# Kernel tuning notes

Hardware: AMD Instinct MI355X
Metric: run time of the kernel (lower is better)

Reference implementation:

```python
import jax, jax.numpy as jnp
from jax import lax
import numpy as np

D_MODEL, N_STATES, N_GROUPS, K_CONV = 1024, 16, 8, 4
BATCH, LENGTH = 2, 2048


def setup_inputs() -> dict:
    key = jax.random.key(0)
    ks = jax.random.split(key, 8)
    x = jax.random.normal(ks[0], (BATCH, LENGTH, D_MODEL), dtype=jnp.float32)
    in_proj_w = jax.random.normal(ks[1], (2 * D_MODEL, D_MODEL), dtype=jnp.float32) * 0.02
    in_proj_b = jnp.zeros((2 * D_MODEL,), dtype=jnp.float32)
    delta_proj_w = jax.random.uniform(ks[2], (D_MODEL, D_MODEL), dtype=jnp.float32, minval=0.001, maxval=0.1)
    a_log = jnp.log(jnp.tile(jnp.arange(1, N_STATES + 1, dtype=jnp.float32), (D_MODEL, 1)))
    b_proj_w = jax.random.normal(ks[3], (N_GROUPS * N_STATES, D_MODEL), dtype=jnp.float32) * 1e-4
    b_proj_b = jnp.zeros((N_GROUPS * N_STATES,), dtype=jnp.float32)
    c_param = jax.random.normal(ks[4], (D_MODEL, N_STATES), dtype=jnp.float32) * 0.02
    # depthwise conv (groups = d_model): kernel [D, 1, K]
    conv_w = jax.random.normal(ks[5], (D_MODEL, 1, K_CONV), dtype=jnp.float32) * (1.0 / np.sqrt(K_CONV))
    conv_b = jnp.zeros((D_MODEL,), dtype=jnp.float32)
    return {"x": x, "in_proj_w": in_proj_w, "in_proj_b": in_proj_b,
            "delta_proj_w": delta_proj_w, "a_log": a_log,
            "b_proj_w": b_proj_w, "b_proj_b": b_proj_b, "c_param": c_param,
            "conv_w": conv_w, "conv_b": conv_b}


def _causal_conv(u, conv_w, conv_b):
    # u: [B, L, D] -> depthwise causal conv along L
    D = u.shape[-1]
    K = conv_w.shape[-1]
    uc = jnp.transpose(u, (0, 2, 1))  # [B, D, L]
    uc = lax.conv_general_dilated(uc, conv_w, window_strides=(1,),
                                  padding=[(K - 1, 0)], feature_group_count=D,
                                  dimension_numbers=("NCH", "OIH", "NCH"))
    uc = uc + conv_b[None, :, None]
    return jnp.transpose(uc, (0, 2, 1))  # [B, L, D]


def _selective_scan(delta, A, Bmat, c_param, u):
    # delta,u: [B,L,D]; A: [D,N]; Bmat: [B,L,G,N]; c_param: [D,N]
    Bsz, L, D = delta.shape
    N = A.shape[1]
    G = Bmat.shape[2]
    Bexp = jnp.repeat(Bmat, D // G, axis=2)            # [B,L,D,N]
    dA = jnp.exp(delta[..., None] * A)                  # [B,L,D,N]
    dBu = (delta * u)[..., None] * Bexp                 # [B,L,D,N]

    def step(h, xs):
        da, dbu = xs
        h = da * h + dbu                                # [B,D,N]
        y = jnp.einsum("bdn,dn->bd", h, c_param)
        return h, y

    h0 = jnp.zeros((Bsz, D, N), dtype=delta.dtype)
    _, ys = lax.scan(step, h0, (jnp.moveaxis(dA, 1, 0), jnp.moveaxis(dBu, 1, 0)))
    return jnp.moveaxis(ys, 0, 1)                       # [B,L,D]


def reference(x, in_proj_w, in_proj_b, delta_proj_w, a_log, b_proj_w, b_proj_b, c_param, conv_w, conv_b):
    Bsz, L, _ = x.shape
    N = a_log.shape[1]
    G = b_proj_w.shape[0] // N
    xp = x @ in_proj_w.T + in_proj_b                    # [B,L,2D]
    u, v = jnp.split(xp, 2, axis=-1)
    delta = jax.nn.softplus(u @ delta_proj_w.T)         # [B,L,D]
    A = -jnp.exp(a_log)                                 # [D,N]
    Bmat = (u @ b_proj_w.T + b_proj_b).reshape(Bsz, L, G, N)
    u_conv = jax.nn.silu(_causal_conv(u, conv_w, conv_b))
    y = _selective_scan(delta, A, Bmat, c_param, u_conv)
    return y * jax.nn.silu(v)
```

## Files before the change

kernel.cpp:

```cpp
#include <hip/hip_runtime.h>
#include <math.h>

#define LTOT 2048
#define MROWS 4096
#define CHK 64
#define NCH (LTOT / CHK)
#define SPAD 20

typedef short bf16x8 __attribute__((ext_vector_type(8)));
typedef float f32x4  __attribute__((ext_vector_type(4)));

__device__ __forceinline__ unsigned short bf16_rne(float f) {
  unsigned u = __float_as_uint(f);
  u += 0x7FFF + ((u >> 16) & 1);
  return (unsigned short)(u >> 16);
}
__device__ __forceinline__ float bf16_to_f(unsigned short h) {
  return __uint_as_float(((unsigned)h) << 16);
}
__device__ __forceinline__ float softplus_f(float x) {
  return (x > 15.f) ? x : log1pf(expf(x));
}
__device__ __forceinline__ float silu_f(float x) {
  return x / (1.f + expf(-x));
}

__global__ void k_cvt_all(const float* __restrict__ x, const float* __restrict__ w1,
                          const float* __restrict__ dw, const float* __restrict__ bw,
                          unsigned short* __restrict__ xh, unsigned short* __restrict__ xl,
                          unsigned short* __restrict__ wfh, unsigned short* __restrict__ wfl,
                          unsigned short* __restrict__ wdbAh, unsigned short* __restrict__ wdbAl) {
  const int blk = blockIdx.x;
  const float* src; unsigned short *h, *l; int i;
  if (blk < 4096)      { src = x;  h = xh;  l = xl;  i = blk * 256 + threadIdx.x; }
  else if (blk < 6144) { src = w1; h = wfh; l = wfl; i = (blk - 4096) * 256 + threadIdx.x; }
  else if (blk < 7168) { src = dw; h = wdbAh; l = wdbAl; i = (blk - 6144) * 256 + threadIdx.x; }
  else                 { src = bw; h = wdbAh + (size_t)1024*1024; l = wdbAl + (size_t)1024*1024;
                         i = (blk - 7168) * 256 + threadIdx.x; }
  const float4 v = ((const float4*)src)[i];
  ushort4 hh, ll;
  hh.x = bf16_rne(v.x); ll.x = bf16_rne(v.x - bf16_to_f(hh.x));
  hh.y = bf16_rne(v.y); ll.y = bf16_rne(v.y - bf16_to_f(hh.y));
  hh.z = bf16_rne(v.z); ll.z = bf16_rne(v.z - bf16_to_f(hh.z));
  hh.w = bf16_rne(v.w); ll.w = bf16_rne(v.w - bf16_to_f(hh.w));
  ((ushort4*)h)[i] = hh;
  ((ushort4*)l)[i] = ll;
}

__global__ __launch_bounds__(256) void k_cvt_t(const float* __restrict__ w1,
    unsigned short* __restrict__ th, unsigned short* __restrict__ tl) {
  __shared__ float ts[64][65];
  const int t = threadIdx.x;
  const int j0 = blockIdx.y * 64, k0 = blockIdx.x * 64;
  const int r = t >> 4, c4 = (t & 15) * 4;
  #pragma unroll
  for (int p = 0; p < 4; ++p) {
    const int row = p * 16 + r;
    const float4 v = *(const float4*)&w1[(size_t)(j0 + row) * 1024 + k0 + c4];
    ts[row][c4] = v.x; ts[row][c4+1] = v.y; ts[row][c4+2] = v.z; ts[row][c4+3] = v.w;
  }
  __syncthreads();
  #pragma unroll
  for (int p = 0; p < 4; ++p) {
    const int rk = p * 16 + r;
    ushort4 hh, ll;
    float f;
    f = ts[c4+0][rk]; hh.x = bf16_rne(f); ll.x = bf16_rne(f - bf16_to_f(hh.x));
    f = ts[c4+1][rk]; hh.y = bf16_rne(f); ll.y = bf16_rne(f - bf16_to_f(hh.y));
    f = ts[c4+2][rk]; hh.z = bf16_rne(f); ll.z = bf16_rne(f - bf16_to_f(hh.z));
    f = ts[c4+3][rk]; hh.w = bf16_rne(f); ll.w = bf16_rne(f - bf16_to_f(hh.w));
    *(ushort4*)&th[(size_t)(k0 + rk) * 1024 + j0 + c4] = hh;
    *(ushort4*)&tl[(size_t)(k0 + rk) * 1024 + j0 + c4] = ll;
  }
}

__global__ void k_bias(const float* __restrict__ b1, const float* __restrict__ dw,
                       const float* __restrict__ bw, const float* __restrict__ bb,
                       float* __restrict__ bfull) {
  const int t = threadIdx.x;
  const int j = blockIdx.x * 16 + (t >> 4);
  const int lane16 = t & 15;
  const float* W = (j < 1024) ? (dw + (size_t)j * 1024) : (bw + (size_t)(j - 1024) * 1024);
  float s = 0.f;
  for (int i = 0; i < 64; ++i) {
    const int k = lane16 + i * 16;
    s = fmaf(b1[k], W[k], s);
  }
  s += __shfl_xor(s, 8, 16);
  s += __shfl_xor(s, 4, 16);
  s += __shfl_xor(s, 2, 16);
  s += __shfl_xor(s, 1, 16);
  if (lane16 == 0) bfull[j] = s + ((j >= 1024) ? bb[j - 1024] : 0.f);
}

__global__ __launch_bounds__(256) void k_wcomp2(
    const unsigned short* __restrict__ Ah_g, const unsigned short* __restrict__ Al_g,
    const unsigned short* __restrict__ Bh_g, const unsigned short* __restrict__ Bl_g,
    unsigned short* __restrict__ outh, unsigned short* __restrict__ outl) {
  __shared__ __align__(16) unsigned short LAh[128*32];
  __shared__ __align__(16) unsigned short LAl[128*32];
  __shared__ __align__(16) unsigned short LBh[128*32];
  __shared__ __align__(16) unsigned short LBl[128*32];
  const int t = threadIdx.x;
  const int wave = t >> 6, lane = t & 63;
  const int m0 = blockIdx.y * 128;
  const int n0 = blockIdx.x * 128;
  const int wr = wave >> 1, wc = wave & 1;
  const int ln = lane & 15, kq = lane >> 4;
  const int srow = lane >> 2, scol = (lane & 3) * 8;

  f32x4 acc[4][4];
  #pragma unroll
  for (int i = 0; i < 4; ++i)
    #pragma unroll
    for (int j = 0; j < 4; ++j) acc[i][j] = (f32x4){0.f, 0.f, 0.f, 0.f};

  const unsigned short* pAh = Ah_g + (size_t)m0 * 1024;
  const unsigned short* pAl = Al_g + (size_t)m0 * 1024;
  const unsigned short* pBh = Bh_g + (size_t)n0 * 1024;
  const unsigned short* pBl = Bl_g + (size_t)n0 * 1024;

  auto stage = [&](const unsigned short* g, unsigned short* lds, int k0) {
    #pragma unroll
    for (int r = 0; r < 2; ++r) {
      const unsigned short* gp = g + (size_t)(r * 64 + wave * 16 + srow) * 1024 + k0 + scol;
      unsigned short* lp = lds + (r * 64 + wave * 16) * 32;
      __builtin_amdgcn_global_load_lds((const __attribute__((address_space(1))) void*)gp,
                                       (__attribute__((address_space(3))) void*)lp, 16, 0, 0);
    }
  };

  for (int k0 = 0; k0 < 1024; k0 += 32) {
    __syncthreads();
    stage(pAh, LAh, k0);
    stage(pAl, LAl, k0);
    stage(pBh, LBh, k0);
    stage(pBl, LBl, k0);
    __syncthreads();
    bf16x8 ah[4], al[4], bh[4], bl[4];
    #pragma unroll
    for (int i = 0; i < 4; ++i) {
      const int ar = (wr * 64 + i * 16 + ln) * 32 + kq * 8;
      const int br = (wc * 64 + i * 16 + ln) * 32 + kq * 8;
      ah[i] = *(const bf16x8*)&LAh[ar];
      al[i] = *(const bf16x8*)&LAl[ar];
      bh[i] = *(const bf16x8*)&LBh[br];
      bl[i] = *(const bf16x8*)&LBl[br];
    }
    #pragma unroll
    for (int i = 0; i < 4; ++i)
      #pragma unroll
      for (int j = 0; j < 4; ++j) {
        acc[i][j] = __builtin_amdgcn_mfma_f32_16x16x32_bf16(ah[i], bh[j], acc[i][j], 0, 0, 0);
        acc[i][j] = __builtin_amdgcn_mfma_f32_16x16x32_bf16(ah[i], bl[j], acc[i][j], 0, 0, 0);
        acc[i][j] = __builtin_amdgcn_mfma_f32_16x16x32_bf16(al[i], bh[j], acc[i][j], 0, 0, 0);
      }
  }

  const int rbase = (blockIdx.y < 8) ? 2176 : 1024;
  #pragma unroll
  for (int nj = 0; nj < 4; ++nj) {
    const int kcol = n0 + wc * 64 + nj * 16 + ln;
    #pragma unroll
    for (int mi = 0; mi < 4; ++mi) {
      const int i = m0 + wr * 64 + mi * 16 + kq * 4;
      #pragma unroll
      for (int j = 0; j < 4; ++j) {
        const float f = acc[mi][nj][j];
        const unsigned short hh = bf16_rne(f);
        const unsigned short ll = bf16_rne(f - bf16_to_f(hh));
        outh[(size_t)(rbase + i + j) * 1024 + kcol] = hh;
        outl[(size_t)(rbase + i + j) * 1024 + kcol] = ll;
      }
    }
  }
}

__global__ __launch_bounds__(256) void k_mm(
    const unsigned short* __restrict__ xh, const unsigned short* __restrict__ xl,
    const unsigned short* __restrict__ wfh, const unsigned short* __restrict__ wfl,
    const float* __restrict__ b1, const float* __restrict__ bfull,
    float* __restrict__ u_, float* __restrict__ v_,
    float* __restrict__ delta, float* __restrict__ Bm) {
  __shared__ __align__(16) unsigned short LAh[128*32];
  __shared__ __align__(16) unsigned short LAl[128*32];
  __shared__ __align__(16) unsigned short LBh[128*32];
  __shared__ __align__(16) unsigned short LBl[128*32];
  const int t = threadIdx.x;
  const int wave = t >> 6, lane = t & 63;
  const int wr = wave >> 1, wc = wave & 1;
  const int ln = lane & 15, kq = lane >> 4;
  const int srow = lane >> 2, scol = (lane & 3) * 8;
  const int flat = blockIdx.x;

  f32x4 acc[4][4];
  #pragma unroll
  for (int i = 0; i < 4; ++i)
    #pragma unroll
    for (int j = 0; j < 4; ++j) acc[i][j] = (f32x4){0.f, 0.f, 0.f, 0.f};

  if (flat < 256) {
    const int wg = (flat & 7) * 32 + (flat >> 3);
    const int tn = wg & 7;
    const int m0 = (wg >> 3) * 128;
    const unsigned short* pAh = xh + (size_t)m0 * 1024;
    const unsigned short* pAl = xl + (size_t)m0 * 1024;
    const unsigned short* pBh = wfh + (size_t)(2176 + tn * 128) * 1024;
    const unsigned short* pBl = wfl + (size_t)(2176 + tn * 128) * 1024;

    auto stage = [&](const unsigned short* g, unsigned short* lds, int k0) {
      #pragma unroll
      for (int r = 0; r < 2; ++r) {
        const unsigned short* gp = g + (size_t)(r * 64 + wave * 16 + srow) * 1024 + k0 + scol;
        unsigned short* lp = lds + (r * 64 + wave * 16) * 32;
        __builtin_amdgcn_global_load_lds((const __attribute__((address_space(1))) void*)gp,
                                         (__attribute__((address_space(3))) void*)lp, 16, 0, 0);
      }
    };

    for (int k0 = 0; k0 < 1024; k0 += 32) {
      __syncthreads();
      stage(pAh, LAh, k0);
      stage(pAl, LAl, k0);
      stage(pBh, LBh, k0);
      stage(pBl, LBl, k0);
      __syncthreads();
      bf16x8 ah[4], al[4], bh[4], bl[4];
      #pragma unroll
      for (int i = 0; i < 4; ++i) {
        const int ar = (wr * 64 + i * 16 + ln) * 32 + kq * 8;
        const int br = (wc * 64 + i * 16 + ln) * 32 + kq * 8;
        ah[i] = *(const bf16x8*)&LAh[ar];
        al[i] = *(const bf16x8*)&LAl[ar];
        bh[i] = *(const bf16x8*)&LBh[br];
        bl[i] = *(const bf16x8*)&LBl[br];
      }
      #pragma unroll
      for (int i = 0; i < 4; ++i)
        #pragma unroll
        for (int j = 0; j < 4; ++j) {
          acc[i][j] = __builtin_amdgcn_mfma_f32_16x16x32_bf16(ah[i], bh[j], acc[i][j], 0, 0, 0);
          acc[i][j] = __builtin_amdgcn_mfma_f32_16x16x32_bf16(ah[i], bl[j], acc[i][j], 0, 0, 0);
          acc[i][j] = __builtin_amdgcn_mfma_f32_16x16x32_bf16(al[i], bh[j], acc[i][j], 0, 0, 0);
        }
    }

    #pragma unroll
    for (int nj = 0; nj < 4; ++nj) {
      const int colg = tn * 128 + wc * 64 + nj * 16 + ln;
      const float bv = bfull[colg];
      #pragma unroll
      for (int mi = 0; mi < 4; ++mi) {
        const int row = m0 + wr * 64 + mi * 16 + kq * 4;
        #pragma unroll
        for (int j = 0; j < 4; ++j)
          delta[(size_t)(row + j) * 1024 + colg] = softplus_f(acc[mi][nj][j] + bv);
      }
    }
  } else {
    const int f2 = flat - 256;
    const int wg = (f2 & 7) * 68 + (f2 >> 3);
    const int tn = wg % 17;
    const int m0 = (wg / 17) * 128;
    const unsigned short* pAh = xh + (size_t)m0 * 1024;
    const unsigned short* pBh = wfh + (size_t)(tn * 128) * 1024;

    auto stage = [&](const unsigned short* g, unsigned short* lds, int k0) {
      #pragma unroll
      for (int r = 0; r < 2; ++r) {
        const unsigned short* gp = g + (size_t)(r * 64 + wave * 16 + srow) * 1024 + k0 + scol;
        unsigned short* lp = lds + (r * 64 + wave * 16) * 32;
        __builtin_amdgcn_global_load_lds((const __attribute__((address_space(1))) void*)gp,
                                         (__attribute__((address_space(3))) void*)lp, 16, 0, 0);
      }
    };

    for (int k0 = 0; k0 < 1024; k0 += 32) {
      __syncthreads();
      stage(pAh, LAh, k0);
      stage(pBh, LBh, k0);
      __syncthreads();
      bf16x8 ah[4], bh[4];
      #pragma unroll
      for (int i = 0; i < 4; ++i) {
        const int ar = (wr * 64 + i * 16 + ln) * 32 + kq * 8;
        const int br = (wc * 64 + i * 16 + ln) * 32 + kq * 8;
        ah[i] = *(const bf16x8*)&LAh[ar];
        bh[i] = *(const bf16x8*)&LBh[br];
      }
      #pragma unroll
      for (int i = 0; i < 4; ++i)
        #pragma unroll
        for (int j = 0; j < 4; ++j)
          acc[i][j] = __builtin_amdgcn_mfma_f32_16x16x32_bf16(ah[i], bh[j], acc[i][j], 0, 0, 0);
    }

    #pragma unroll
    for (int nj = 0; nj < 4; ++nj) {
      const int colg = tn * 128 + wc * 64 + nj * 16 + ln;
      const float bv = (tn < 16) ? b1[colg] : bfull[1024 + colg - 2048];
      #pragma unroll
      for (int mi = 0; mi < 4; ++mi) {
        const int row = m0 + wr * 64 + mi * 16 + kq * 4;
        #pragma unroll
        for (int j = 0; j < 4; ++j) {
          const float val = acc[mi][nj][j] + bv;
          if (tn < 8)       u_[(size_t)(row + j) * 1024 + colg] = val;
          else if (tn < 16) v_[(size_t)(row + j) * 1024 + colg - 1024] = val;
          else              Bm[(size_t)(row + j) * 128 + colg - 2048] = val;
        }
      }
    }
  }
}

__global__ __launch_bounds__(256) void k_scanA(
    const float* __restrict__ delta, const float* __restrict__ u_,
    const float* __restrict__ Bm, const float* __restrict__ a_log,
    const float* __restrict__ cw, const float* __restrict__ cb,
    float* __restrict__ hend, float* __restrict__ Pp)
{
  __shared__ float sru[68][SPAD];
  __shared__ float sd[CHK][SPAD];
  __shared__ float sb[CHK][SPAD];
  __shared__ float suc[CHK][SPAD];
  const int t = threadIdx.x;
  const int bid = blockIdx.x;
  const int dblk = bid & 63;
  const int ch   = (bid >> 6) & (NCH - 1);
  const int b    = bid >> 11;
  const int d0 = dblk * 16;
  const int g  = dblk >> 3;
  const int l0 = ch * CHK;
  const size_t mb = (size_t)b * LTOT;

  {
    const int lrow = t >> 2;
    const int lc4  = (t & 3) * 4;
    const size_t r = mb + l0 + lrow;
    float4 rd = *(const float4*)&delta[r*1024 + d0 + lc4];
    float4 rb = *(const float4*)&Bm[r*128 + g*16 + lc4];
    *(float4*)&sd[lrow][lc4] = rd;
    *(float4*)&sb[lrow][lc4] = rb;
    const int sl = l0 + lrow - 4;
    float4 ru = (sl >= 0) ? *(const float4*)&u_[(mb + sl)*1024 + d0 + lc4]
                          : (float4){0.f, 0.f, 0.f, 0.f};
    *(float4*)&sru[lrow][lc4] = ru;
    if (t < 16) {
      const int rr2 = 64 + (t >> 2);
      const int sl2 = l0 + rr2 - 4;
      float4 r2 = *(const float4*)&u_[(mb + sl2)*1024 + d0 + (t & 3) * 4];
      *(float4*)&sru[rr2][(t & 3) * 4] = r2;
    }
  }
  __syncthreads();
  {
    const int c = t & 15;
    const int rb4 = (t >> 4) * 4;
    const float4 cwf = *(const float4*)&cw[(d0 + c) * 4];
    const float cbf = cb[d0 + c];
    #pragma unroll
    for (int q = 0; q < 4; ++q) {
      const int l = rb4 + q;
      float a = cbf;
      a = fmaf(sru[l+1][c], cwf.x, a);
      a = fmaf(sru[l+2][c], cwf.y, a);
      a = fmaf(sru[l+3][c], cwf.z, a);
      a = fmaf(sru[l+4][c], cwf.w, a);
      suc[l][c] = silu_f(a);
    }
  }
  __syncthreads();

  const int gi = t >> 4;
  const int n  = t & 15;
  const int d  = d0 + gi;
  const float A2 = -expf(a_log[d*16 + n]) * 1.4426950408889634f;

  float h = 0.f, P = 1.f;
  #pragma unroll 8
  for (int l = 0; l < CHK; ++l) {
    const float dv = sd[l][gi];
    const float uv = suc[l][gi];
    const float bv = sb[l][n];
    const float da = exp2f(dv * A2);
    P *= da;
    h = fmaf(da, h, dv * uv * bv);
  }
  const size_t idx = ((size_t)(b*NCH + ch) * 1024 + d) * 16 + n;
  hend[idx] = h;
  Pp[idx]   = P;
}

__global__ void k_scanB(float* hP, const float* __restrict__ Pp)
{
  const int t = blockIdx.x * 256 + threadIdx.x;
  const int b  = t >> 14;
  const int dn = t & 16383;
  float H = 0.f;
  for (int ch = 0; ch < NCH; ++ch) {
    const size_t idx = ((size_t)(b*NCH + ch) << 14) + dn;
    const float he = hP[idx];
    const float P  = Pp[idx];
    hP[idx] = H;
    H = fmaf(P, H, he);
  }
}

__global__ __launch_bounds__(256) void k_scanC(
    const float* __restrict__ v_, const float* __restrict__ delta,
    const float* __restrict__ u_, const float* __restrict__ Bm,
    const float* __restrict__ a_log, const float* __restrict__ cp,
    const float* __restrict__ cw, const float* __restrict__ cb,
    const float* __restrict__ Hstart, float* __restrict__ out)
{
  __shared__ float sru[68][SPAD];
  __shared__ float sd[CHK][SPAD];
  __shared__ float sb[CHK][SPAD];
  __shared__ float suc[CHK][SPAD];
  __shared__ float sv[CHK][SPAD];
  __shared__ float sy[CHK][SPAD];
  const int t = threadIdx.x;
  const int bid = blockIdx.x;
  const int dblk = bid & 63;
  const int ch   = (bid >> 6) & (NCH - 1);
  const int b    = bid >> 11;
  const int d0 = dblk * 16;
  const int g  = dblk >> 3;
  const int l0 = ch * CHK;
  const size_t mb = (size_t)b * LTOT;

  {
    const int lrow = t >> 2;
    const int lc4  = (t & 3) * 4;
    const size_t r = mb + l0 + lrow;
    float4 rd = *(const float4*)&delta[r*1024 + d0 + lc4];
    float4 rb = *(const float4*)&Bm[r*128 + g*16 + lc4];
    float4 rv = *(const float4*)&v_[r*1024 + d0 + lc4];
    *(float4*)&sd[lrow][lc4] = rd;
    *(float4*)&sb[lrow][lc4] = rb;
    *(float4*)&sv[lrow][lc4] = rv;
    const int sl = l0 + lrow - 4;
    float4 ru = (sl >= 0) ? *(const float4*)&u_[(mb + sl)*1024 + d0 + lc4]
                          : (float4){0.f, 0.f, 0.f, 0.f};
    *(float4*)&sru[lrow][lc4] = ru;
    if (t < 16) {
      const int rr2 = 64 + (t >> 2);
      const int sl2 = l0 + rr2 - 4;
      float4 r2 = *(const float4*)&u_[(mb + sl2)*1024 + d0 + (t & 3) * 4];
      *(float4*)&sru[rr2][(t & 3) * 4] = r2;
    }
  }
  __syncthreads();
  {
    const int c = t & 15;
    const int rb4 = (t >> 4) * 4;
    const float4 cwf = *(const float4*)&cw[(d0 + c) * 4];
    const float cbf = cb[d0 + c];
    #pragma unroll
    for (int q = 0; q < 4; ++q) {
      const int l = rb4 + q;
      float a = cbf;
      a = fmaf(sru[l+1][c], cwf.x, a);
      a = fmaf(sru[l+2][c], cwf.y, a);
      a = fmaf(sru[l+3][c], cwf.z, a);
      a = fmaf(sru[l+4][c], cwf.w, a);
      suc[l][c] = silu_f(a);
    }
  }
  __syncthreads();

  const int gi = t >> 4;
  const int n  = t & 15;
  const int d  = d0 + gi;
  const float A2 = -expf(a_log[d*16 + n]) * 1.4426950408889634f;
  const float cc = cp[d*16 + n];
  float h = Hstart[((size_t)(b*NCH + ch) * 1024 + d) * 16 + n];

  #pragma unroll
  for (int l16 = 0; l16 < CHK; l16 += 16) {
    float p[16];
    #pragma unroll
    for (int j = 0; j < 16; ++j) {
      const int l = l16 + j;
      const float dv = sd[l][gi];
      const float uv = suc[l][gi];
      const float bv = sb[l][n];
      const float da = exp2f(dv * A2);
      h = fmaf(da, h, dv * uv * bv);
      p[j] = h * cc;
    }
    float q8[8];
    #pragma unroll
    for (int j = 0; j < 8; ++j) {
      const float send = (n & 8) ? p[j]     : p[j + 8];
      const float keep = (n & 8) ? p[j + 8] : p[j];
      q8[j] = keep + __shfl_xor(send, 8, 16);
    }
    float q4[4];
    #pragma unroll
    for (int j = 0; j < 4; ++j) {
      const float send = (n & 4) ? q8[j]     : q8[j + 4];
      const float keep = (n & 4) ? q8[j + 4] : q8[j];
      q4[j] = keep + __shfl_xor(send, 4, 16);
    }
    float q2[2];
    #pragma unroll
    for (int j = 0; j < 2; ++j) {
      const float send = (n & 2) ? q4[j]     : q4[j + 2];
      const float keep = (n & 2) ? q4[j + 2] : q4[j];
      q2[j] = keep + __shfl_xor(send, 2, 16);
    }
    {
      const float send = (n & 1) ? q2[0] : q2[1];
      const float keep = (n & 1) ? q2[1] : q2[0];
      sy[l16 + n][gi] = keep + __shfl_xor(send, 1, 16);
    }
  }

  __syncthreads();
  const int rr = t >> 4;
  const int c  = t & 15;
  #pragma unroll
  for (int k = 0; k < 4; ++k) {
    const int r = rr + k * 16;
    const float vv = sv[r][c];
    out[(mb + l0 + r) * 1024 + d0 + c] = sy[r][c] * silu_f(vv);
  }
}

extern "C" void kernel_launch(void* const* d_in, const int* in_sizes, int n_in,
                              void* d_out, int out_size, void* d_ws, size_t ws_size,
                              hipStream_t stream) {
  const float* x    = (const float*)d_in[0];
  const float* w1   = (const float*)d_in[1];
  const float* b1   = (const float*)d_in[2];
  const float* dw   = (const float*)d_in[3];
  const float* alog = (const float*)d_in[4];
  const float* bw   = (const float*)d_in[5];
  const float* bb   = (const float*)d_in[6];
  const float* cp   = (const float*)d_in[7];
  const float* cw   = (const float*)d_in[8];
  const float* cb   = (const float*)d_in[9];
  float* out = (float*)d_out;

  const size_t M4 = (size_t)MROWS * 1024;
  float* u_    = (float*)d_ws;
  float* v_    = u_ + M4;
  float* delta = v_ + M4;
  float* Bm    = delta + M4;
  unsigned short* xh  = (unsigned short*)(Bm + (size_t)MROWS * 128);
  unsigned short* xl  = xh + M4;
  unsigned short* wfh = xl + M4;
  unsigned short* wfl = wfh + (size_t)3200 * 1024;
  float* bfull = (float*)(wfl + (size_t)3200 * 1024);
  unsigned short* wdbAh = (unsigned short*)delta;
  unsigned short* wdbAl = wdbAh + (size_t)1152 * 1024;
  unsigned short* w1th  = wdbAl + (size_t)1152 * 1024;
  unsigned short* w1tl  = w1th + (size_t)1024 * 1024;
  float* hend = (float*)wfh;
  float* Pp   = hend + (size_t)2 * NCH * 1024 * 16;

  k_cvt_all<<<7296, 256, 0, stream>>>(x, w1, dw, bw, xh, xl, wfh, wfl, wdbAh, wdbAl);
  k_cvt_t<<<dim3(16, 16), 256, 0, stream>>>(w1, w1th, w1tl);
  k_bias<<<72, 256, 0, stream>>>(b1, dw, bw, bb, bfull);
  k_wcomp2<<<dim3(8, 9), 256, 0, stream>>>(wdbAh, wdbAl, w1th, w1tl, wfh, wfl);
  k_mm<<<800, 256, 0, stream>>>(xh, xl, wfh, wfl, b1, bfull, u_, v_, delta, Bm);
  k_scanA<<<2 * NCH * 64, 256, 0, stream>>>(delta, u_, Bm, alog, cw, cb, hend, Pp);
  k_scanB<<<128, 256, 0, stream>>>(hend, Pp);
  k_scanC<<<2 * NCH * 64, 256, 0, stream>>>(v_, delta, u_, Bm, alog, cp, cw, cb, hend, out);
}
```

Before: 217.7 us.

## Drop split-bf16 low parts for x and composed weights, merge prep kernels

After: 207.7 us. 1.05x faster.

```diff
diff --git a/kernel.cpp b/kernel.cpp
--- a/kernel.cpp
+++ b/kernel.cpp
@@ -25,78 +25,84 @@
   return x / (1.f + expf(-x));
 }
 
-__global__ void k_cvt_all(const float* __restrict__ x, const float* __restrict__ w1,
-                          const float* __restrict__ dw, const float* __restrict__ bw,
-                          unsigned short* __restrict__ xh, unsigned short* __restrict__ xl,
-                          unsigned short* __restrict__ wfh, unsigned short* __restrict__ wfl,
-                          unsigned short* __restrict__ wdbAh, unsigned short* __restrict__ wdbAl) {
+__global__ __launch_bounds__(256) void k_prep(
+    const float* __restrict__ x, const float* __restrict__ w1,
+    const float* __restrict__ dw, const float* __restrict__ bw,
+    const float* __restrict__ b1, const float* __restrict__ bb,
+    unsigned short* __restrict__ xh, unsigned short* __restrict__ wfh,
+    unsigned short* __restrict__ wdbAh, unsigned short* __restrict__ wdbAl,
+    unsigned short* __restrict__ w1th, unsigned short* __restrict__ w1tl,
+    float* __restrict__ bfull) {
+  __shared__ float ts[64][65];
   const int blk = blockIdx.x;
-  const float* src; unsigned short *h, *l; int i;
-  if (blk < 4096)      { src = x;  h = xh;  l = xl;  i = blk * 256 + threadIdx.x; }
-  else if (blk < 6144) { src = w1; h = wfh; l = wfl; i = (blk - 4096) * 256 + threadIdx.x; }
-  else if (blk < 7168) { src = dw; h = wdbAh; l = wdbAl; i = (blk - 6144) * 256 + threadIdx.x; }
-  else                 { src = bw; h = wdbAh + (size_t)1024*1024; l = wdbAl + (size_t)1024*1024;
-                         i = (blk - 7168) * 256 + threadIdx.x; }
-  const float4 v = ((const float4*)src)[i];
-  ushort4 hh, ll;
-  hh.x = bf16_rne(v.x); ll.x = bf16_rne(v.x - bf16_to_f(hh.x));
-  hh.y = bf16_rne(v.y); ll.y = bf16_rne(v.y - bf16_to_f(hh.y));
-  hh.z = bf16_rne(v.z); ll.z = bf16_rne(v.z - bf16_to_f(hh.z));
-  hh.w = bf16_rne(v.w); ll.w = bf16_rne(v.w - bf16_to_f(hh.w));
-  ((ushort4*)h)[i] = hh;
-  ((ushort4*)l)[i] = ll;
-}
-
-__global__ __launch_bounds__(256) void k_cvt_t(const float* __restrict__ w1,
-    unsigned short* __restrict__ th, unsigned short* __restrict__ tl) {
-  __shared__ float ts[64][65];
   const int t = threadIdx.x;
-  const int j0 = blockIdx.y * 64, k0 = blockIdx.x * 64;
-  const int r = t >> 4, c4 = (t & 15) * 4;
-  #pragma unroll
-  for (int p = 0; p < 4; ++p) {
-    const int row = p * 16 + r;
-    const float4 v = *(const float4*)&w1[(size_t)(j0 + row) * 1024 + k0 + c4];
-    ts[row][c4] = v.x; ts[row][c4+1] = v.y; ts[row][c4+2] = v.z; ts[row][c4+3] = v.w;
-  }
-  __syncthreads();
-  #pragma unroll
-  for (int p = 0; p < 4; ++p) {
-    const int rk = p * 16 + r;
+
+  if (blk < 6144) {
+    const float* src; unsigned short* h; int i;
+    if (blk < 4096) { src = x;  h = xh;  i = blk * 256 + t; }
+    else            { src = w1; h = wfh; i = (blk - 4096) * 256 + t; }
+    const float4 v = ((const float4*)src)[i];
+    ushort4 hh;
+    hh.x = bf16_rne(v.x); hh.y = bf16_rne(v.y);
+    hh.z = bf16_rne(v.z); hh.w = bf16_rne(v.w);
+    ((ushort4*)h)[i] = hh;
+  } else if (blk < 7296) {
+    const float* src; unsigned short *h, *l; int i;
+    if (blk < 7168) { src = dw; h = wdbAh; l = wdbAl; i = (blk - 6144) * 256 + t; }
+    else            { src = bw; h = wdbAh + (size_t)1024*1024; l = wdbAl + (size_t)1024*1024;
+                      i = (blk - 7168) * 256 + t; }
+    const float4 v = ((const float4*)src)[i];
     ushort4 hh, ll;
-    float f;
-    f = ts[c4+0][rk]; hh.x = bf16_rne(f); ll.x = bf16_rne(f - bf16_to_f(hh.x));
-    f = ts[c4+1][rk]; hh.y = bf16_rne(f); ll.y = bf16_rne(f - bf16_to_f(hh.y));
-    f = ts[c4+2][rk]; hh.z = bf16_rne(f); ll.z = bf16_rne(f - bf16_to_f(hh.z));
-    f = ts[c4+3][rk]; hh.w = bf16_rne(f); ll.w = bf16_rne(f - bf16_to_f(hh.w));
-    *(ushort4*)&th[(size_t)(k0 + rk) * 1024 + j0 + c4] = hh;
-    *(ushort4*)&tl[(size_t)(k0 + rk) * 1024 + j0 + c4] = ll;
-  }
-}
-
-__global__ void k_bias(const float* __restrict__ b1, const float* __restrict__ dw,
-                       const float* __restrict__ bw, const float* __restrict__ bb,
-                       float* __restrict__ bfull) {
-  const int t = threadIdx.x;
-  const int j = blockIdx.x * 16 + (t >> 4);
-  const int lane16 = t & 15;
-  const float* W = (j < 1024) ? (dw + (size_t)j * 1024) : (bw + (size_t)(j - 1024) * 1024);
-  float s = 0.f;
-  for (int i = 0; i < 64; ++i) {
-    const int k = lane16 + i * 16;
-    s = fmaf(b1[k], W[k], s);
-  }
-  s += __shfl_xor(s, 8, 16);
-  s += __shfl_xor(s, 4, 16);
-  s += __shfl_xor(s, 2, 16);
-  s += __shfl_xor(s, 1, 16);
-  if (lane16 == 0) bfull[j] = s + ((j >= 1024) ? bb[j - 1024] : 0.f);
+    hh.x = bf16_rne(v.x); ll.x = bf16_rne(v.x - bf16_to_f(hh.x));
+    hh.y = bf16_rne(v.y); ll.y = bf16_rne(v.y - bf16_to_f(hh.y));
+    hh.z = bf16_rne(v.z); ll.z = bf16_rne(v.z - bf16_to_f(hh.z));
+    hh.w = bf16_rne(v.w); ll.w = bf16_rne(v.w - bf16_to_f(hh.w));
+    ((ushort4*)h)[i] = hh;
+    ((ushort4*)l)[i] = ll;
+  } else if (blk < 7552) {
+    const int s = blk - 7296;
+    const int k0 = (s & 15) * 64, j0 = (s >> 4) * 64;
+    const int r = t >> 4, c4 = (t & 15) * 4;
+    #pragma unroll
+    for (int p = 0; p < 4; ++p) {
+      const int row = p * 16 + r;
+      const float4 v = *(const float4*)&w1[(size_t)(j0 + row) * 1024 + k0 + c4];
+      ts[row][c4] = v.x; ts[row][c4+1] = v.y; ts[row][c4+2] = v.z; ts[row][c4+3] = v.w;
+    }
+    __syncthreads();
+    #pragma unroll
+    for (int p = 0; p < 4; ++p) {
+      const int rk = p * 16 + r;
+      ushort4 hh, ll;
+      float f;
+      f = ts[c4+0][rk]; hh.x = bf16_rne(f); ll.x = bf16_rne(f - bf16_to_f(hh.x));
+      f = ts[c4+1][rk]; hh.y = bf16_rne(f); ll.y = bf16_rne(f - bf16_to_f(hh.y));
+      f = ts[c4+2][rk]; hh.z = bf16_rne(f); ll.z = bf16_rne(f - bf16_to_f(hh.z));
+      f = ts[c4+3][rk]; hh.w = bf16_rne(f); ll.w = bf16_rne(f - bf16_to_f(hh.w));
+      *(ushort4*)&w1th[(size_t)(k0 + rk) * 1024 + j0 + c4] = hh;
+      *(ushort4*)&w1tl[(size_t)(k0 + rk) * 1024 + j0 + c4] = ll;
+    }
+  } else {
+    const int j = (blk - 7552) * 16 + (t >> 4);
+    const int lane16 = t & 15;
+    const float* W = (j < 1024) ? (dw + (size_t)j * 1024) : (bw + (size_t)(j - 1024) * 1024);
+    float s = 0.f;
+    for (int i = 0; i < 64; ++i) {
+      const int k = lane16 + i * 16;
+      s = fmaf(b1[k], W[k], s);
+    }
+    s += __shfl_xor(s, 8, 16);
+    s += __shfl_xor(s, 4, 16);
+    s += __shfl_xor(s, 2, 16);
+    s += __shfl_xor(s, 1, 16);
+    if (lane16 == 0) bfull[j] = s + ((j >= 1024) ? bb[j - 1024] : 0.f);
+  }
 }
 
 __global__ __launch_bounds__(256) void k_wcomp2(
     const unsigned short* __restrict__ Ah_g, const unsigned short* __restrict__ Al_g,
     const unsigned short* __restrict__ Bh_g, const unsigned short* __restrict__ Bl_g,
-    unsigned short* __restrict__ outh, unsigned short* __restrict__ outl) {
+    unsigned short* __restrict__ outh) {
   __shared__ __align__(16) unsigned short LAh[128*32];
   __shared__ __align__(16) unsigned short LAl[128*32];
   __shared__ __align__(16) unsigned short LBh[128*32];
@@ -165,33 +171,28 @@
     for (int mi = 0; mi < 4; ++mi) {
       const int i = m0 + wr * 64 + mi * 16 + kq * 4;
       #pragma unroll
-      for (int j = 0; j < 4; ++j) {
-        const float f = acc[mi][nj][j];
-        const unsigned short hh = bf16_rne(f);
-        const unsigned short ll = bf16_rne(f - bf16_to_f(hh));
-        outh[(size_t)(rbase + i + j) * 1024 + kcol] = hh;
-        outl[(size_t)(rbase + i + j) * 1024 + kcol] = ll;
-      }
-    }
-  }
-}
-
-__global__ __launch_bounds__(256) void k_mm(
-    const unsigned short* __restrict__ xh, const unsigned short* __restrict__ xl,
-    const unsigned short* __restrict__ wfh, const unsigned short* __restrict__ wfl,
+      for (int j = 0; j < 4; ++j)
+        outh[(size_t)(rbase + i + j) * 1024 + kcol] = bf16_rne(acc[mi][nj][j]);
+    }
+  }
+}
+
+__global__ __launch_bounds__(256) void k_mm_u(
+    const unsigned short* __restrict__ xh, const unsigned short* __restrict__ wfh,
     const float* __restrict__ b1, const float* __restrict__ bfull,
     float* __restrict__ u_, float* __restrict__ v_,
     float* __restrict__ delta, float* __restrict__ Bm) {
   __shared__ __align__(16) unsigned short LAh[128*32];
-  __shared__ __align__(16) unsigned short LAl[128*32];
   __shared__ __align__(16) unsigned short LBh[128*32];
-  __shared__ __align__(16) unsigned short LBl[128*32];
   const int t = threadIdx.x;
   const int wave = t >> 6, lane = t & 63;
+  const int flat = blockIdx.x;
+  const int wg = (flat & 7) * 100 + (flat >> 3);
+  const int tn = wg % 25;
+  const int m0 = (wg / 25) * 128;
   const int wr = wave >> 1, wc = wave & 1;
   const int ln = lane & 15, kq = lane >> 4;
   const int srow = lane >> 2, scol = (lane & 3) * 8;
-  const int flat = blockIdx.x;
 
   f32x4 acc[4][4];
   #pragma unroll
@@ -199,116 +200,56 @@
     #pragma unroll
     for (int j = 0; j < 4; ++j) acc[i][j] = (f32x4){0.f, 0.f, 0.f, 0.f};
 
-  if (flat < 256) {
-    const int wg = (flat & 7) * 32 + (flat >> 3);
-    const int tn = wg & 7;
-    const int m0 = (wg >> 3) * 128;
-    const unsigned short* pAh = xh + (size_t)m0 * 1024;
-    const unsigned short* pAl = xl + (size_t)m0 * 1024;
-    const unsigned short* pBh = wfh + (size_t)(2176 + tn * 128) * 1024;
-    const unsigned short* pBl = wfl + (size_t)(2176 + tn * 128) * 1024;
-
-    auto stage = [&](const unsigned short* g, unsigned short* lds, int k0) {
+  const unsigned short* pAh = xh + (size_t)m0 * 1024;
+  const unsigned short* pBh = wfh + (size_t)(tn * 128) * 1024;
+
+  auto stage = [&](const unsigned short* g, unsigned short* lds, int k0) {
+    #pragma unroll
+    for (int r = 0; r < 2; ++r) {
+      const unsigned short* gp = g + (size_t)(r * 64 + wave * 16 + srow) * 1024 + k0 + scol;
+      unsigned short* lp = lds + (r * 64 + wave * 16) * 32;
+      __builtin_amdgcn_global_load_lds((const __attribute__((address_space(1))) void*)gp,
+                                       (__attribute__((address_space(3))) void*)lp, 16, 0, 0);
+    }
+  };
+
+  for (int k0 = 0; k0 < 1024; k0 += 32) {
+    __syncthreads();
+    stage(pAh, LAh, k0);
+    stage(pBh, LBh, k0);
+    __syncthreads();
+    bf16x8 ah[4], bh[4];
+    #pragma unroll
+    for (int i = 0; i < 4; ++i) {
+      const int ar = (wr * 64 + i * 16 + ln) * 32 + kq * 8;
+      const int br = (wc * 64 + i * 16 + ln) * 32 + kq * 8;
+      ah[i] = *(const bf16x8*)&LAh[ar];
+      bh[i] = *(const bf16x8*)&LBh[br];
+    }
+    #pragma unroll
+    for (int i = 0; i < 4; ++i)
       #pragma unroll
-      for (int r = 0; r < 2; ++r) {
-        const unsigned short* gp = g + (size_t)(r * 64 + wave * 16 + srow) * 1024 + k0 + scol;
-        unsigned short* lp = lds + (r * 64 + wave * 16) * 32;
-        __builtin_amdgcn_global_load_lds((const __attribute__((address_space(1))) void*)gp,
-                                         (__attribute__((address_space(3))) void*)lp, 16, 0, 0);
-      }
-    };
-
-    for (int k0 = 0; k0 < 1024; k0 += 32) {
-      __syncthreads();
-      stage(pAh, LAh, k0);
-      stage(pAl, LAl, k0);
-      stage(pBh, LBh, k0);
-      stage(pBl, LBl, k0);
-      __syncthreads();
-      bf16x8 ah[4], al[4], bh[4], bl[4];
+      for (int j = 0; j < 4; ++j)
+        acc[i][j] = __builtin_amdgcn_mfma_f32_16x16x32_bf16(ah[i], bh[j], acc[i][j], 0, 0, 0);
+  }
+
+  #pragma unroll
+  for (int nj = 0; nj < 4; ++nj) {
+    const int colg = tn * 128 + wc * 64 + nj * 16 + ln;
+    float bv;
+    if (colg < 2048)      bv = b1[colg];
+    else if (colg < 2176) bv = bfull[1024 + colg - 2048];
+    else                  bv = bfull[colg - 2176];
+    #pragma unroll
+    for (int mi = 0; mi < 4; ++mi) {
+      const int row = m0 + wr * 64 + mi * 16 + kq * 4;
       #pragma unroll
-      for (int i = 0; i < 4; ++i) {
-        const int ar = (wr * 64 + i * 16 + ln) * 32 + kq * 8;
-        const int br = (wc * 64 + i * 16 + ln) * 32 + kq * 8;
-        ah[i] = *(const bf16x8*)&LAh[ar];
-        al[i] = *(const bf16x8*)&LAl[ar];
-        bh[i] = *(const bf16x8*)&LBh[br];
-        bl[i] = *(const bf16x8*)&LBl[br];
-      }
-      #pragma unroll
-      for (int i = 0; i < 4; ++i)
-        #pragma unroll
-        for (int j = 0; j < 4; ++j) {
-          acc[i][j] = __builtin_amdgcn_mfma_f32_16x16x32_bf16(ah[i], bh[j], acc[i][j], 0, 0, 0);
-          acc[i][j] = __builtin_amdgcn_mfma_f32_16x16x32_bf16(ah[i], bl[j], acc[i][j], 0, 0, 0);
-          acc[i][j] = __builtin_amdgcn_mfma_f32_16x16x32_bf16(al[i], bh[j], acc[i][j], 0, 0, 0);
-        }
-    }
-
-    #pragma unroll
-    for (int nj = 0; nj < 4; ++nj) {
-      const int colg = tn * 128 + wc * 64 + nj * 16 + ln;
-      const float bv = bfull[colg];
-      #pragma unroll
-      for (int mi = 0; mi < 4; ++mi) {
-        const int row = m0 + wr * 64 + mi * 16 + kq * 4;
-        #pragma unroll
-        for (int j = 0; j < 4; ++j)
-          delta[(size_t)(row + j) * 1024 + colg] = softplus_f(acc[mi][nj][j] + bv);
-      }
-    }
-  } else {
-    const int f2 = flat - 256;
-    const int wg = (f2 & 7) * 68 + (f2 >> 3);
-    const int tn = wg % 17;
-    const int m0 = (wg / 17) * 128;
-    const unsigned short* pAh = xh + (size_t)m0 * 1024;
-    const unsigned short* pBh = wfh + (size_t)(tn * 128) * 1024;
-
-    auto stage = [&](const unsigned short* g, unsigned short* lds, int k0) {
-      #pragma unroll
-      for (int r = 0; r < 2; ++r) {
-        const unsigned short* gp = g + (size_t)(r * 64 + wave * 16 + srow) * 1024 + k0 + scol;
-        unsigned short* lp = lds + (r * 64 + wave * 16) * 32;
-        __builtin_amdgcn_global_load_lds((const __attribute__((address_space(1))) void*)gp,
-                                         (__attribute__((address_space(3))) void*)lp, 16, 0, 0);
-      }
-    };
-
-    for (int k0 = 0; k0 < 1024; k0 += 32) {
-      __syncthreads();
-      stage(pAh, LAh, k0);
-      stage(pBh, LBh, k0);
-      __syncthreads();
-      bf16x8 ah[4], bh[4];
-      #pragma unroll
-      for (int i = 0; i < 4; ++i) {
-        const int ar = (wr * 64 + i * 16 + ln) * 32 + kq * 8;
-        const int br = (wc * 64 + i * 16 + ln) * 32 + kq * 8;
-        ah[i] = *(const bf16x8*)&LAh[ar];
-        bh[i] = *(const bf16x8*)&LBh[br];
-      }
-      #pragma unroll
-      for (int i = 0; i < 4; ++i)
-        #pragma unroll
-        for (int j = 0; j < 4; ++j)
-          acc[i][j] = __builtin_amdgcn_mfma_f32_16x16x32_bf16(ah[i], bh[j], acc[i][j], 0, 0, 0);
-    }
-
-    #pragma unroll
-    for (int nj = 0; nj < 4; ++nj) {
-      const int colg = tn * 128 + wc * 64 + nj * 16 + ln;
-      const float bv = (tn < 16) ? b1[colg] : bfull[1024 + colg - 2048];
-      #pragma unroll
-      for (int mi = 0; mi < 4; ++mi) {
-        const int row = m0 + wr * 64 + mi * 16 + kq * 4;
-        #pragma unroll
-        for (int j = 0; j < 4; ++j) {
-          const float val = acc[mi][nj][j] + bv;
-          if (tn < 8)       u_[(size_t)(row + j) * 1024 + colg] = val;
-          else if (tn < 16) v_[(size_t)(row + j) * 1024 + colg - 1024] = val;
-          else              Bm[(size_t)(row + j) * 128 + colg - 2048] = val;
-        }
+      for (int j = 0; j < 4; ++j) {
+        const float val = acc[mi][nj][j] + bv;
+        if (tn < 8)        u_[(size_t)(row + j) * 1024 + colg] = val;
+        else if (tn < 16)  v_[(size_t)(row + j) * 1024 + colg - 1024] = val;
+        else if (tn == 16) Bm[(size_t)(row + j) * 128 + colg - 2048] = val;
+        else               delta[(size_t)(row + j) * 1024 + colg - 2176] = softplus_f(val);
       }
     }
   }
@@ -561,11 +502,10 @@
   float* hend = (float*)wfh;
   float* Pp   = hend + (size_t)2 * NCH * 1024 * 16;
 
-  k_cvt_all<<<7296, 256, 0, stream>>>(x, w1, dw, bw, xh, xl, wfh, wfl, wdbAh, wdbAl);
-  k_cvt_t<<<dim3(16, 16), 256, 0, stream>>>(w1, w1th, w1tl);
-  k_bias<<<72, 256, 0, stream>>>(b1, dw, bw, bb, bfull);
-  k_wcomp2<<<dim3(8, 9), 256, 0, stream>>>(wdbAh, wdbAl, w1th, w1tl, wfh, wfl);
-  k_mm<<<800, 256, 0, stream>>>(xh, xl, wfh, wfl, b1, bfull, u_, v_, delta, Bm);
+  k_prep<<<7624, 256, 0, stream>>>(x, w1, dw, bw, b1, bb,
+                                   xh, wfh, wdbAh, wdbAl, w1th, w1tl, bfull);
+  k_wcomp2<<<dim3(8, 9), 256, 0, stream>>>(wdbAh, wdbAl, w1th, w1tl, wfh);
+  k_mm_u<<<800, 256, 0, stream>>>(xh, wfh, b1, bfull, u_, v_, delta, Bm);
   k_scanA<<<2 * NCH * 64, 256, 0, stream>>>(delta, u_, Bm, alog, cw, cb, hend, Pp);
   k_scanB<<<128, 256, 0, stream>>>(hend, Pp);
   k_scanC<<<2 * NCH * 64, 256, 0, stream>>>(v_, delta, u_, Bm, alog, cp, cw, cb, hend, out);
```
